# Kernel optimization log

Hardware: AMD Instinct MI355X
Metric: run time of the kernel (lower is better)

## Reference

```python
import jax, jax.numpy as jnp
from jax import lax
import numpy as np

H = 16        # hidden_size == input_size
L = 8         # num_layers


def _lstm_layer(x_seq, Wih, Whh, bih, bhh):
    # x_seq: [B, T, H] -> outputs [B, T, H]; PyTorch gate order i,f,g,o
    B = x_seq.shape[0]
    b = bih + bhh  # [4H]

    def step(carry, xt):
        h, c = carry
        gates = xt @ Wih.T + h @ Whh.T + b  # [B, 4H]
        i, f, g, o = jnp.split(gates, 4, axis=-1)
        c = jax.nn.sigmoid(f) * c + jax.nn.sigmoid(i) * jnp.tanh(g)
        h = jax.nn.sigmoid(o) * jnp.tanh(c)
        return (h, c), h

    h0 = jnp.zeros((B, H), x_seq.dtype)
    (_, _), hs = lax.scan(step, (h0, h0), jnp.swapaxes(x_seq, 0, 1))
    return jnp.swapaxes(hs, 0, 1)  # [B, T, H]


def setup_inputs() -> dict:
    key = jax.random.key(0)
    ks = jax.random.split(key, 9)
    s = 1.0 / np.sqrt(H)  # PyTorch default init scale
    x = jax.random.normal(ks[0], (2048, 512, H), dtype=jnp.float32)
    W_ih = jax.random.uniform(ks[1], (L, 4 * H, H), jnp.float32, -s, s)
    W_hh = jax.random.uniform(ks[2], (L, 4 * H, H), jnp.float32, -s, s)
    b_ih = jax.random.uniform(ks[3], (L, 4 * H), jnp.float32, -s, s)
    b_hh = jax.random.uniform(ks[4], (L, 4 * H), jnp.float32, -s, s)
    Wp = jax.random.uniform(ks[5], (3, H), jnp.float32, -s, s)
    bp = jax.random.uniform(ks[6], (3,), jnp.float32, -s, s)
    Wo = jax.random.uniform(ks[7], (3, H), jnp.float32, -s, s)
    bo = jax.random.uniform(ks[8], (3,), jnp.float32, -s, s)
    return {"x": x, "W_ih": W_ih, "W_hh": W_hh, "b_ih": b_ih, "b_hh": b_hh,
            "Wp": Wp, "bp": bp, "Wo": Wo, "bo": bo}


def reference(x, W_ih, W_hh, b_ih, b_hh, Wp, bp, Wo, bo):
    h = x
    for l in range(L):  # fixed small layer count
        h = _lstm_layer(h, W_ih[l], W_hh[l], b_ih[l], b_hh[l])
    last = h[:, -1, :]                       # [B, H]
    position = last @ Wp.T + bp              # [B, 3]
    orientation = jnp.tanh(last @ Wo.T + bo) # [B, 3]
    return jnp.concatenate((position, orientation), axis=1)  # [B, 6]
```

## Files before the change

### kernel.cpp

```cpp
#include <hip/hip_runtime.h>
#include <math.h>

typedef _Float16 f16x8 __attribute__((ext_vector_type(8)));
typedef _Float16 f16x2 __attribute__((ext_vector_type(2)));
typedef float    f32x4 __attribute__((ext_vector_type(4)));

constexpr int kT    = 512;
constexpr int kH    = 16;
constexpr int kL    = 8;
constexpr int kG    = 64;
constexpr int kNB   = 8;
constexpr int kPad  = 24;
constexpr int kRows = 9;
constexpr int kSlots= 16;
constexpr int kLyr  = kL + 1;
constexpr int kSE   = kLyr * kRows * kPad;
constexpr int kIters= 33;

constexpr float kL2E = 1.4426950408889634f;

__device__ __forceinline__ float swz8(float v) {
    return __int_as_float(__builtin_amdgcn_ds_swizzle(__float_as_int(v), 0x201F));
}
__device__ __forceinline__ float sigm2(float z) {
    return __builtin_amdgcn_rcpf(1.0f + __builtin_amdgcn_exp2f(z));
}
__device__ __forceinline__ void cbar() { asm volatile("" ::: "memory"); }

__global__ __launch_bounds__(512, 2)
void lstm_async(const float* __restrict__ x,
                const float* __restrict__ Wih, const float* __restrict__ Whh,
                const float* __restrict__ bih, const float* __restrict__ bhh,
                const float* __restrict__ Wp,  const float* __restrict__ bpos,
                const float* __restrict__ Wo,  const float* __restrict__ bori,
                float* __restrict__ out)
{
    const int tid  = threadIdx.x;
    const int l    = tid >> 6;
    const int lane = tid & 63;
    const int n    = lane & 15;
    const int q    = lane >> 4;
    const int bn   = n & 7;
    const bool cLow = (n < 8);
    const bool bact = ((q >> 1) == (n >> 3));

    __shared__ __align__(16) _Float16 hb[kSlots][kLyr][kRows][kPad];
    __shared__ int cnt[kL];

    {
        int* hz = (int*)&hb[0][0][0][0];
        for (int i = tid; i < (int)(sizeof(hb) / 4); i += 512) hz[i] = 0;
        if (tid < kL) cnt[tid] = -1;
    }

    auto loadA = [&](const float* W, int rLow, int rHigh) -> f16x8 {
        const int row = (q < 2) ? (rLow + n) : (rHigh + n);
        const float* src = W + (size_t)l * kG * kH + row * kH + (q & 1) * 8;
        f16x8 a;
        #pragma unroll
        for (int j = 0; j < 8; ++j) a[j] = (_Float16)src[j];
        return a;
    };
    const f16x8 A1P1 = loadA(Wih, 0, 16), A2P1 = loadA(Whh, 0, 16);
    const f16x8 A1P2 = loadA(Wih, 32, 48), A2P2 = loadA(Whh, 32, 48);

    float abk1[4], abk2[4];
    const float ank2 = cLow ? (-2.0f * kL2E) : (-kL2E);
    const float am2  = cLow ? 2.0f : 1.0f;
    const float ams2 = cLow ? -1.0f : 0.0f;
    #pragma unroll
    for (int r = 0; r < 4; ++r) {
        const int u  = q * 4 + r;
        const int g1 = l * kG + (cLow ? u : 16 + u);
        const int g2 = l * kG + (cLow ? 32 + u : 48 + u);
        abk1[r] = -kL2E * (bih[g1] + bhh[g1]);
        abk2[r] = ank2  * (bih[g2] + bhh[g2]);
    }

    const int boff = (bact ? bn * kPad : 8 * kPad) + (q & 1) * 8;
    const _Float16* b1b = &hb[0][l    ][0][0] + boff;
    const _Float16* b2b = &hb[0][l + 1][0][0] + boff;
    _Float16* hwb = &hb[0][l + 1][bn][q * 4 + (cLow ? 0 : 2)];
    _Float16* xwb = &hb[0][0][lane >> 3][(lane & 7) * 2];

    const float* xg_ptr =
        x + ((size_t)(blockIdx.x * kNB + (lane >> 3)) * kT) * kH + (lane & 7) * 2;
    float xg0 = 0.f, xg1 = 0.f;
    if (l == 0) {
        float2 v0 = *(const float2*)(xg_ptr);
        hb[15][0][lane >> 3][(lane & 7) * 2]     = (_Float16)v0.x;
        hb[15][0][lane >> 3][(lane & 7) * 2 + 1] = (_Float16)v0.y;
        float2 v1 = *(const float2*)(xg_ptr + kH);
        xg0 = v1.x; xg1 = v1.y;
    }

    float c0 = 0.f, c1 = 0.f;
    __syncthreads();

    const f32x4 zeroC = {0.f, 0.f, 0.f, 0.f};
    volatile const int* upc = (l > 0)      ? &cnt[l - 1] : nullptr;
    volatile const int* dnc = (l < kL - 1) ? &cnt[l + 1] : nullptr;

    for (int it = 0; it < kIters; ++it) {
        const int sb = it * 16;
        #pragma unroll
        for (int k = 0; k < 16; ++k) {
            const int s = sb + k;

            if ((k & 1) == 0 && l > 0) {
                while (*upc < s) __builtin_amdgcn_s_sleep(1);
                cbar();
            }
            if ((k == 0 || k == 8) && l < kL - 1) {
                const int need = (k == 0) ? (sb - 8) : sb;
                while (*dnc < need) __builtin_amdgcn_s_sleep(1);
                cbar();
            }

            const int  t      = s - l;
            const bool active = ((unsigned)t < (unsigned)kT);
            const int  rs     = (k + 15) & 15;

            const f16x8 B1 = *(const f16x8*)(b1b + rs * kSE);
            const f16x8 B2 = *(const f16x8*)(b2b + rs * kSE);

            f32x4 d1 = __builtin_amdgcn_mfma_f32_16x16x32_f16(A2P1, B2, zeroC, 0, 0, 0);
            f32x4 d2 = __builtin_amdgcn_mfma_f32_16x16x32_f16(A2P2, B2, zeroC, 0, 0, 0);
            d1 = __builtin_amdgcn_mfma_f32_16x16x32_f16(A1P1, B1, d1, 0, 0, 0);
            d2 = __builtin_amdgcn_mfma_f32_16x16x32_f16(A1P2, B1, d2, 0, 0, 0);

            float p1s[4], p2s[4];
            #pragma unroll
            for (int r = 0; r < 4; ++r)
                p1s[r] = sigm2(fmaf(-kL2E, d1[r], abk1[r]));
            #pragma unroll
            for (int r = 0; r < 4; ++r)
                p2s[r] = fmaf(am2, sigm2(fmaf(ank2, d2[r], abk2[r])), ams2);

            float hh[2];
            float cc[2] = {c0, c1};
            #pragma unroll
            for (int kk = 0; kk < 2; ++kk) {
                const float T1 = cLow ? p1s[kk + 2] : p1s[kk];
                const float R1 = swz8(T1);
                const float iv = cLow ? p1s[kk] : R1;
                const float fv = cLow ? R1 : p1s[kk + 2];
                const float T2 = cLow ? p2s[kk + 2] : p2s[kk];
                const float R2 = swz8(T2);
                const float gv = cLow ? p2s[kk] : R2;
                const float ov = cLow ? R2 : p2s[kk + 2];

                float cn = fmaf(fv, cc[kk], iv * gv);
                cn = active ? cn : 0.0f;
                cc[kk] = cn;
                const float tc = fmaf(2.0f, sigm2(-2.0f * kL2E * cn), -1.0f);
                hh[kk] = ov * tc;
            }
            c0 = cc[0]; c1 = cc[1];

            f16x2 hp = { (_Float16)hh[0], (_Float16)hh[1] };
            *(f16x2*)(hwb + k * kSE) = hp;

            if (l == 0) {
                _Float16* xw = xwb + k * kSE;
                xw[0] = (_Float16)xg0;
                xw[1] = (_Float16)xg1;
                int tn = s + 2; if (tn > kT - 1) tn = kT - 1;
                float2 v = *(const float2*)(xg_ptr + (size_t)tn * kH);
                xg0 = v.x; xg1 = v.y;
            }

            if (k & 1) {
                cbar();
                if (lane == 0) *(volatile int*)&cnt[l] = s;
            }
        }
    }

    __syncthreads();

    if (l == kL - 1) {
        const int bb = lane >> 3;
        const int r  = lane & 7;
        if (r < 6) {
            const bool  isP   = (r < 3);
            const float* wrow = isP ? (Wp + r * kH) : (Wo + (r - 3) * kH);
            float acc = isP ? bpos[r] : bori[r - 3];
            #pragma unroll
            for (int u = 0; u < kH; ++u)
                acc = fmaf((float)hb[6][kL][bb][u], wrow[u], acc);
            if (!isP) acc = fmaf(2.0f, sigm2(-2.0f * kL2E * acc), -1.0f);
            out[(size_t)(blockIdx.x * kNB + bb) * 6 + r] = acc;
        }
    }
}

extern "C" void kernel_launch(void* const* d_in, const int* in_sizes, int n_in,
                              void* d_out, int out_size, void* d_ws, size_t ws_size,
                              hipStream_t stream) {
    const float* x    = (const float*)d_in[0];
    const float* Wih  = (const float*)d_in[1];
    const float* Whh  = (const float*)d_in[2];
    const float* bih  = (const float*)d_in[3];
    const float* bhh  = (const float*)d_in[4];
    const float* Wp   = (const float*)d_in[5];
    const float* bpos = (const float*)d_in[6];
    const float* Wo   = (const float*)d_in[7];
    const float* bori = (const float*)d_in[8];
    float* out = (float*)d_out;

    const int B = in_sizes[0] / (kT * kH);
    lstm_async<<<dim3(B / kNB), dim3(512), 0, stream>>>(x, Wih, Whh, bih, bhh,
                                                        Wp, bpos, Wo, bori, out);
}
```

Measured before the change: 331.0 us.

## Map two LSTM layers per wavefront to halve waves and cross-wave syncs

Each wavefront now processes a pair of adjacent LSTM layers (4 waves of 256 threads instead of 8 waves of 512), interleaving the two layers' MFMA and activation chains within one step. This cuts the number of inter-wave spin-wait handshakes and lets the two independent dependency chains fill latency with instruction-level parallelism in a single wave. The loop is restructured into 8-step blocks over the 16-slot ring buffer, with the wait on the downstream wave done once per block. The trade-off is roughly doubled serial work per wave per step and one wave per SIMD, so latency hiding between waves is lost.

```diff
diff --git a/kernel.cpp b/kernel.cpp
--- a/kernel.cpp
+++ b/kernel.cpp
@@ -15,7 +15,8 @@
 constexpr int kSlots= 16;
 constexpr int kLyr  = kL + 1;
 constexpr int kSE   = kLyr * kRows * kPad;
-constexpr int kIters= 33;
+constexpr int kNW   = 4;
+constexpr int kIB   = 65;
 
 constexpr float kL2E = 1.4426950408889634f;
 
@@ -27,33 +28,35 @@
 }
 __device__ __forceinline__ void cbar() { asm volatile("" ::: "memory"); }
 
-__global__ __launch_bounds__(512, 2)
-void lstm_async(const float* __restrict__ x,
-                const float* __restrict__ Wih, const float* __restrict__ Whh,
-                const float* __restrict__ bih, const float* __restrict__ bhh,
-                const float* __restrict__ Wp,  const float* __restrict__ bpos,
-                const float* __restrict__ Wo,  const float* __restrict__ bori,
-                float* __restrict__ out)
+__global__ __launch_bounds__(256, 1)
+void lstm_pair(const float* __restrict__ x,
+               const float* __restrict__ Wih, const float* __restrict__ Whh,
+               const float* __restrict__ bih, const float* __restrict__ bhh,
+               const float* __restrict__ Wp,  const float* __restrict__ bpos,
+               const float* __restrict__ Wo,  const float* __restrict__ bori,
+               float* __restrict__ out)
 {
     const int tid  = threadIdx.x;
-    const int l    = tid >> 6;
+    const int w    = tid >> 6;
     const int lane = tid & 63;
     const int n    = lane & 15;
     const int q    = lane >> 4;
     const int bn   = n & 7;
     const bool cLow = (n < 8);
     const bool bact = ((q >> 1) == (n >> 3));
+    const int lA   = 2 * w;
+    const int lB   = 2 * w + 1;
 
     __shared__ __align__(16) _Float16 hb[kSlots][kLyr][kRows][kPad];
-    __shared__ int cnt[kL];
+    __shared__ int cnt[kNW];
 
     {
         int* hz = (int*)&hb[0][0][0][0];
-        for (int i = tid; i < (int)(sizeof(hb) / 4); i += 512) hz[i] = 0;
-        if (tid < kL) cnt[tid] = -1;
-    }
-
-    auto loadA = [&](const float* W, int rLow, int rHigh) -> f16x8 {
+        for (int i = tid; i < (int)(sizeof(hb) / 4); i += 256) hz[i] = 0;
+        if (tid < kNW) cnt[tid] = -1;
+    }
+
+    auto loadA = [&](const float* W, int l, int rLow, int rHigh) -> f16x8 {
         const int row = (q < 2) ? (rLow + n) : (rHigh + n);
         const float* src = W + (size_t)l * kG * kH + row * kH + (q & 1) * 8;
         f16x8 a;
@@ -61,32 +64,41 @@
         for (int j = 0; j < 8; ++j) a[j] = (_Float16)src[j];
         return a;
     };
-    const f16x8 A1P1 = loadA(Wih, 0, 16), A2P1 = loadA(Whh, 0, 16);
-    const f16x8 A1P2 = loadA(Wih, 32, 48), A2P2 = loadA(Whh, 32, 48);
-
-    float abk1[4], abk2[4];
+    const f16x8 A1P1a = loadA(Wih, lA, 0, 16), A2P1a = loadA(Whh, lA, 0, 16);
+    const f16x8 A1P2a = loadA(Wih, lA, 32, 48), A2P2a = loadA(Whh, lA, 32, 48);
+    const f16x8 A1P1b = loadA(Wih, lB, 0, 16), A2P1b = loadA(Whh, lB, 0, 16);
+    const f16x8 A1P2b = loadA(Wih, lB, 32, 48), A2P2b = loadA(Whh, lB, 32, 48);
+
     const float ank2 = cLow ? (-2.0f * kL2E) : (-kL2E);
     const float am2  = cLow ? 2.0f : 1.0f;
     const float ams2 = cLow ? -1.0f : 0.0f;
+    float abk1a[4], abk2a[4], abk1b[4], abk2b[4];
     #pragma unroll
     for (int r = 0; r < 4; ++r) {
-        const int u  = q * 4 + r;
-        const int g1 = l * kG + (cLow ? u : 16 + u);
-        const int g2 = l * kG + (cLow ? 32 + u : 48 + u);
-        abk1[r] = -kL2E * (bih[g1] + bhh[g1]);
-        abk2[r] = ank2  * (bih[g2] + bhh[g2]);
+        const int u = q * 4 + r;
+        const int g1a = lA * kG + (cLow ? u : 16 + u);
+        const int g2a = lA * kG + (cLow ? 32 + u : 48 + u);
+        const int g1b = lB * kG + (cLow ? u : 16 + u);
+        const int g2b = lB * kG + (cLow ? 32 + u : 48 + u);
+        abk1a[r] = -kL2E * (bih[g1a] + bhh[g1a]);
+        abk2a[r] = ank2  * (bih[g2a] + bhh[g2a]);
+        abk1b[r] = -kL2E * (bih[g1b] + bhh[g1b]);
+        abk2b[r] = ank2  * (bih[g2b] + bhh[g2b]);
     }
 
     const int boff = (bact ? bn * kPad : 8 * kPad) + (q & 1) * 8;
-    const _Float16* b1b = &hb[0][l    ][0][0] + boff;
-    const _Float16* b2b = &hb[0][l + 1][0][0] + boff;
-    _Float16* hwb = &hb[0][l + 1][bn][q * 4 + (cLow ? 0 : 2)];
-    _Float16* xwb = &hb[0][0][lane >> 3][(lane & 7) * 2];
+    const _Float16* b1a = &hb[0][lA    ][0][0] + boff;
+    const _Float16* b2a = &hb[0][lA + 1][0][0] + boff;
+    const _Float16* b1b = &hb[0][lB    ][0][0] + boff;
+    const _Float16* b2b = &hb[0][lB + 1][0][0] + boff;
+    _Float16* hwa = &hb[0][lA + 1][bn][q * 4 + (cLow ? 0 : 2)];
+    _Float16* hwb = &hb[0][lB + 1][bn][q * 4 + (cLow ? 0 : 2)];
+    _Float16* xw  = &hb[0][0][lane >> 3][(lane & 7) * 2];
 
     const float* xg_ptr =
         x + ((size_t)(blockIdx.x * kNB + (lane >> 3)) * kT) * kH + (lane & 7) * 2;
     float xg0 = 0.f, xg1 = 0.f;
-    if (l == 0) {
+    if (w == 0) {
         float2 v0 = *(const float2*)(xg_ptr);
         hb[15][0][lane >> 3][(lane & 7) * 2]     = (_Float16)v0.x;
         hb[15][0][lane >> 3][(lane & 7) * 2 + 1] = (_Float16)v0.y;
@@ -94,92 +106,102 @@
         xg0 = v1.x; xg1 = v1.y;
     }
 
-    float c0 = 0.f, c1 = 0.f;
+    float c0a = 0.f, c1a = 0.f, c0b = 0.f, c1b = 0.f;
     __syncthreads();
 
     const f32x4 zeroC = {0.f, 0.f, 0.f, 0.f};
-    volatile const int* upc = (l > 0)      ? &cnt[l - 1] : nullptr;
-    volatile const int* dnc = (l < kL - 1) ? &cnt[l + 1] : nullptr;
-
-    for (int it = 0; it < kIters; ++it) {
-        const int sb = it * 16;
-        #pragma unroll
-        for (int k = 0; k < 16; ++k) {
+    volatile const int* upc = (w > 0)       ? &cnt[w - 1] : nullptr;
+    volatile const int* dnc = (w < kNW - 1) ? &cnt[w + 1] : nullptr;
+
+    auto lstep = [&](const f16x8& A1P1, const f16x8& A2P1,
+                     const f16x8& A1P2, const f16x8& A2P2,
+                     const float* abk1, const float* abk2,
+                     const _Float16* b1, const _Float16* b2, _Float16* hw,
+                     float& c0, float& c1, int roff, int woff, bool active) {
+        const f16x8 B1 = *(const f16x8*)(b1 + roff);
+        const f16x8 B2 = *(const f16x8*)(b2 + roff);
+        f32x4 d1 = __builtin_amdgcn_mfma_f32_16x16x32_f16(A2P1, B2, zeroC, 0, 0, 0);
+        f32x4 d2 = __builtin_amdgcn_mfma_f32_16x16x32_f16(A2P2, B2, zeroC, 0, 0, 0);
+        d1 = __builtin_amdgcn_mfma_f32_16x16x32_f16(A1P1, B1, d1, 0, 0, 0);
+        d2 = __builtin_amdgcn_mfma_f32_16x16x32_f16(A1P2, B1, d2, 0, 0, 0);
+
+        float p1s[4], p2s[4];
+        #pragma unroll
+        for (int r = 0; r < 4; ++r)
+            p1s[r] = sigm2(fmaf(-kL2E, d1[r], abk1[r]));
+        #pragma unroll
+        for (int r = 0; r < 4; ++r)
+            p2s[r] = fmaf(am2, sigm2(fmaf(ank2, d2[r], abk2[r])), ams2);
+
+        float hh[2];
+        float cc[2] = {c0, c1};
+        #pragma unroll
+        for (int kk = 0; kk < 2; ++kk) {
+            const float T1 = cLow ? p1s[kk + 2] : p1s[kk];
+            const float R1 = swz8(T1);
+            const float iv = cLow ? p1s[kk] : R1;
+            const float fv = cLow ? R1 : p1s[kk + 2];
+            const float T2 = cLow ? p2s[kk + 2] : p2s[kk];
+            const float R2 = swz8(T2);
+            const float gv = cLow ? p2s[kk] : R2;
+            const float ov = cLow ? R2 : p2s[kk + 2];
+            float cn = fmaf(fv, cc[kk], iv * gv);
+            cn = active ? cn : 0.0f;
+            cc[kk] = cn;
+            const float tc = fmaf(2.0f, sigm2(-2.0f * kL2E * cn), -1.0f);
+            hh[kk] = ov * tc;
+        }
+        c0 = cc[0]; c1 = cc[1];
+        f16x2 hp = { (_Float16)hh[0], (_Float16)hh[1] };
+        *(f16x2*)(hw + woff) = hp;
+    };
+
+    #pragma unroll 1
+    for (int ib = 0; ib < kIB; ++ib) {
+        const int sb  = ib * 8;
+        const int sbm = sb & 15;
+        const int wb  = sbm * kSE;
+        const int rb0 = ((sbm ^ 8) + 7) * kSE;
+
+        if (w < kNW - 1) {
+            while (*dnc < sb - 8) __builtin_amdgcn_s_sleep(1);
+            cbar();
+        }
+        #pragma unroll
+        for (int k = 0; k < 8; ++k) {
             const int s = sb + k;
-
-            if ((k & 1) == 0 && l > 0) {
+            if ((k & 1) == 0 && w > 0) {
                 while (*upc < s) __builtin_amdgcn_s_sleep(1);
                 cbar();
             }
-            if ((k == 0 || k == 8) && l < kL - 1) {
-                const int need = (k == 0) ? (sb - 8) : sb;
-                while (*dnc < need) __builtin_amdgcn_s_sleep(1);
-                cbar();
-            }
-
-            const int  t      = s - l;
-            const bool active = ((unsigned)t < (unsigned)kT);
-            const int  rs     = (k + 15) & 15;
-
-            const f16x8 B1 = *(const f16x8*)(b1b + rs * kSE);
-            const f16x8 B2 = *(const f16x8*)(b2b + rs * kSE);
-
-            f32x4 d1 = __builtin_amdgcn_mfma_f32_16x16x32_f16(A2P1, B2, zeroC, 0, 0, 0);
-            f32x4 d2 = __builtin_amdgcn_mfma_f32_16x16x32_f16(A2P2, B2, zeroC, 0, 0, 0);
-            d1 = __builtin_amdgcn_mfma_f32_16x16x32_f16(A1P1, B1, d1, 0, 0, 0);
-            d2 = __builtin_amdgcn_mfma_f32_16x16x32_f16(A1P2, B1, d2, 0, 0, 0);
-
-            float p1s[4], p2s[4];
-            #pragma unroll
-            for (int r = 0; r < 4; ++r)
-                p1s[r] = sigm2(fmaf(-kL2E, d1[r], abk1[r]));
-            #pragma unroll
-            for (int r = 0; r < 4; ++r)
-                p2s[r] = fmaf(am2, sigm2(fmaf(ank2, d2[r], abk2[r])), ams2);
-
-            float hh[2];
-            float cc[2] = {c0, c1};
-            #pragma unroll
-            for (int kk = 0; kk < 2; ++kk) {
-                const float T1 = cLow ? p1s[kk + 2] : p1s[kk];
-                const float R1 = swz8(T1);
-                const float iv = cLow ? p1s[kk] : R1;
-                const float fv = cLow ? R1 : p1s[kk + 2];
-                const float T2 = cLow ? p2s[kk + 2] : p2s[kk];
-                const float R2 = swz8(T2);
-                const float gv = cLow ? p2s[kk] : R2;
-                const float ov = cLow ? R2 : p2s[kk + 2];
-
-                float cn = fmaf(fv, cc[kk], iv * gv);
-                cn = active ? cn : 0.0f;
-                cc[kk] = cn;
-                const float tc = fmaf(2.0f, sigm2(-2.0f * kL2E * cn), -1.0f);
-                hh[kk] = ov * tc;
-            }
-            c0 = cc[0]; c1 = cc[1];
-
-            f16x2 hp = { (_Float16)hh[0], (_Float16)hh[1] };
-            *(f16x2*)(hwb + k * kSE) = hp;
-
-            if (l == 0) {
-                _Float16* xw = xwb + k * kSE;
-                xw[0] = (_Float16)xg0;
-                xw[1] = (_Float16)xg1;
+            const int roff = (k == 0) ? rb0 : (wb + (k - 1) * kSE);
+            const int woff = wb + k * kSE;
+            const bool actA = ((unsigned)(s - lA) < (unsigned)kT);
+            const bool actB = ((unsigned)(s - lB) < (unsigned)kT);
+
+            lstep(A1P1a, A2P1a, A1P2a, A2P2a, abk1a, abk2a,
+                  b1a, b2a, hwa, c0a, c1a, roff, woff, actA);
+            lstep(A1P1b, A2P1b, A1P2b, A2P2b, abk1b, abk2b,
+                  b1b, b2b, hwb, c0b, c1b, roff, woff, actB);
+
+            if (w == 0) {
+                _Float16* xq = xw + woff;
+                xq[0] = (_Float16)xg0;
+                xq[1] = (_Float16)xg1;
                 int tn = s + 2; if (tn > kT - 1) tn = kT - 1;
                 float2 v = *(const float2*)(xg_ptr + (size_t)tn * kH);
                 xg0 = v.x; xg1 = v.y;
             }
-
             if (k & 1) {
                 cbar();
-                if (lane == 0) *(volatile int*)&cnt[l] = s;
+                if (lane == 0) *(volatile int*)&cnt[w] = s;
             }
         }
     }
 
     __syncthreads();
 
-    if (l == kL - 1) {
+    if (w == kNW - 1) {
         const int bb = lane >> 3;
         const int r  = lane & 7;
         if (r < 6) {
@@ -210,6 +232,6 @@
     float* out = (float*)d_out;
 
     const int B = in_sizes[0] / (kT * kH);
-    lstm_async<<<dim3(B / kNB), dim3(512), 0, stream>>>(x, Wih, Whh, bih, bhh,
-                                                        Wp, bpos, Wo, bori, out);
-}
+    lstm_pair<<<dim3(B / kNB), dim3(256), 0, stream>>>(x, Wih, Whh, bih, bhh,
+                                                       Wp, bpos, Wo, bori, out);
+}
```

Result: slower. 427.6 us (+29.2%).
